# Performance work log

Hardware: AMD Instinct MI355X
Metric: run time of the kernel (lower is better)

The kernel has to match this reference:

```python
import math
import jax, jax.numpy as jnp
import numpy as np

NLAT, NLON = 61, 120
C, H = 64, 4
DH = C // H
HID = 128
NSEG = NLAT * NLON  # number of grid points / softmax segments
EPS = 1e-6
SCALE = 1.0 / math.sqrt(DH)


def _build_geometry():
    """Neighbor pairs within theta_cutoff on the equiangular (pole-including) grid.

    The neighborhood structure is longitude-shift invariant, so we enumerate it
    for output longitude 0 and replicate with a modular longitude shift.
    """
    nlat, nlon = NLAT, NLON
    theta = np.pi * np.arange(nlat) / (nlat - 1)           # colatitudes incl. poles
    lam = 2.0 * np.pi * np.arange(nlon) / nlon
    theta_cutoff = 7.0 / math.sqrt(math.pi) * math.pi / (nlat - 1)
    ct, st = np.cos(theta), np.sin(theta)
    # great-circle distance between (theta_o, 0) and (theta_i, dlon): [nlat, nlat, nlon]
    cosd = (ct[:, None, None] * ct[None, :, None]
            + st[:, None, None] * st[None, :, None] * np.cos(lam)[None, None, :])
    dist = np.arccos(np.clip(cosd, -1.0, 1.0))
    ho, hi, dl = np.nonzero(dist <= theta_cutoff)          # E reference-column entries
    wo = np.arange(nlon)
    out_idx = (ho[:, None] * nlon + wo[None, :]).reshape(-1).astype(np.int32)
    in_idx = (hi[:, None] * nlon + (dl[:, None] + wo[None, :]) % nlon).reshape(-1).astype(np.int32)
    # quadrature (integration) weights: sin(theta) measure, zero at the poles
    w = (st * (np.pi / (nlat - 1)) * (2.0 * np.pi / nlon)).astype(np.float32)
    quad_w = np.repeat(w, nlon)                            # [NSEG]
    return jnp.asarray(out_idx), jnp.asarray(in_idx), jnp.asarray(quad_w)


def setup_inputs() -> dict:
    key = jax.random.key(0)
    ks = jax.random.split(key, 8)
    out_idx, in_idx, quad_w = _build_geometry()

    def w(k, shape, fan_in):
        return jax.random.normal(k, shape, dtype=jnp.float32) / np.float32(np.sqrt(fan_in))

    return {
        "x": jax.random.normal(ks[0], (1, C, NLAT, NLON), dtype=jnp.float32),
        "wq": w(ks[1], (C, C), C),
        "wk": w(ks[2], (C, C), C),
        "wv": w(ks[3], (C, C), C),
        "wo": w(ks[4], (C, C), C),
        "w1": w(ks[5], (HID, C), C),
        "b1": jnp.zeros((HID,), jnp.float32),
        "w2": w(ks[6], (C, HID), HID),
        "b2": jnp.zeros((C,), jnp.float32),
        "ln0_g": jnp.ones((C,), jnp.float32),
        "ln0_b": jnp.zeros((C,), jnp.float32),
        "ln1_g": jnp.ones((C,), jnp.float32),
        "ln1_b": jnp.zeros((C,), jnp.float32),
        "quad_w": quad_w,
        "out_idx": out_idx,
        "in_idx": in_idx,
    }


def _layernorm(x, g, b):
    # channel-wise LayerNorm at every spatial location; x: [B, C, H, W]
    m = jnp.mean(x, axis=1, keepdims=True)
    v = jnp.mean((x - m) ** 2, axis=1, keepdims=True)
    xh = (x - m) * jax.lax.rsqrt(v + EPS)
    return xh * g[None, :, None, None] + b[None, :, None, None]


def _neighborhood_attn(x, wq, wk, wv, wo, quad_w, out_idx, in_idx):
    # x: [B, C, nlat, nlon] (fp32)
    B = x.shape[0]
    q = jnp.einsum('oc,bchw->bohw', wq, x).reshape(B, H, DH, NSEG)
    k = jnp.einsum('oc,bchw->bohw', wk, x).reshape(B, H, DH, NSEG)
    v = jnp.einsum('oc,bchw->bohw', wv, x).reshape(B, H, DH, NSEG)
    qg = q[..., out_idx]                                   # [B,H,DH,NNZ]
    kg = k[..., in_idx]
    s = jnp.einsum('bhdn,bhdn->bhn', qg, kg) * SCALE       # [B,H,NNZ]
    s = jnp.moveaxis(s, -1, 0)                             # [NNZ,B,H]
    smax = jax.ops.segment_max(s, out_idx, num_segments=NSEG)
    # quadrature-weighted, numerically stable softmax over each neighborhood
    alpha = jnp.exp(s - smax[out_idx]) * quad_w[in_idx][:, None, None]
    vg = jnp.moveaxis(v[..., in_idx], -1, 0)               # [NNZ,B,H,DH]
    num = jax.ops.segment_sum(alpha[..., None] * vg, out_idx, num_segments=NSEG)
    den = jax.ops.segment_sum(alpha, out_idx, num_segments=NSEG)
    att = num / den[..., None]                             # [NSEG,B,H,DH]
    att = jnp.moveaxis(att, 0, -1).reshape(B, C, NLAT, NLON)
    return jnp.einsum('oc,bchw->bohw', wo, att)


def reference(x, wq, wk, wv, wo, w1, b1, w2, b2, ln0_g, ln0_b, ln1_g, ln1_b,
              quad_w, out_idx, in_idx):
    residual = x
    h0 = _layernorm(x, ln0_g, ln0_b)
    a = _neighborhood_attn(h0.astype(jnp.float32), wq, wk, wv, wo,
                           quad_w, out_idx, in_idx).astype(x.dtype)
    x1 = a + residual
    h1 = _layernorm(x1, ln1_g, ln1_b)
    m = jax.nn.gelu(jnp.einsum('fc,bchw->bfhw', w1, h1) + b1[None, :, None, None],
                    approximate=False)
    m = jnp.einsum('cf,bfhw->bchw', w2, m) + b2[None, :, None, None]
    return m + x1
```

## Files before the change

### kernel.cpp

```cpp
#include <hip/hip_runtime.h>
#include <math.h>

#define NSEG 7320
#define NLON 120
#define HIDN 128
#define ZSPL 6
#define ECHUNK 8
#define NCHUNK 96

__global__ __launch_bounds__(256) void z0_zero(float4* __restrict__ p, int n4)
{
    int i = blockIdx.x * 256 + threadIdx.x;
    if (i < n4) p[i] = make_float4(0.f, 0.f, 0.f, 0.f);
}

__global__ __launch_bounds__(64) void k1_ln_qkv(
    const float* __restrict__ x,  const float* __restrict__ wq,
    const float* __restrict__ wk, const float* __restrict__ wv,
    const float* __restrict__ g,  const float* __restrict__ b,
    const int* __restrict__ out_idx, const int* __restrict__ in_idx,
    const float* __restrict__ qw, int E,
    float* __restrict__ q_pl, float* __restrict__ k_pl, float* __restrict__ v_pl,
    int* __restrict__ row_start, int4* __restrict__ meta)
{
    const int lane = threadIdx.x;
    const int tile = blockIdx.x;
    const int grp  = blockIdx.y;

    if (grp >= 24) {
        for (int e = tile * 64 + lane; e < E; e += 115 * 64) {
            int ho = out_idx[e * NLON] / NLON;
            if (e == 0) {
                row_start[ho] = 0;
            } else {
                int hp = out_idx[(e - 1) * NLON] / NLON;
                if (hp != ho) row_start[ho] = e;
            }
            if (e == E - 1) row_start[ho + 1] = E;
            int i0 = in_idx[e * NLON];
            int hi = i0 / NLON;
            int dl = i0 - hi * NLON;
            meta[e] = make_int4(hi * NLON, dl, __float_as_int(qw[i0]), ho);
        }
        return;
    }

    const int n = tile * 64 + lane;
    if (n >= NSEG) return;

    float xv[64];
    float s = 0.f, s2 = 0.f;
#pragma unroll
    for (int c = 0; c < 64; ++c) { float t = x[c * NSEG + n]; xv[c] = t; s += t; s2 += t * t; }
    float mean = s * 0.015625f;
    float var  = s2 * 0.015625f - mean * mean;
    float rstd = rsqrtf(var + 1e-6f);
#pragma unroll
    for (int c = 0; c < 64; ++c) xv[c] = (xv[c] - mean) * rstd * g[c] + b[c];

    const int mm    = grp >> 3;
    const int obase = (grp & 7) * 8;
    const float* __restrict__ w = (mm == 0) ? wq : (mm == 1) ? wk : wv;
    float* __restrict__ dst = (mm == 0) ? q_pl : (mm == 1) ? k_pl : v_pl;
    const float scale = (mm == 0) ? 0.25f : 1.0f;

#pragma unroll
    for (int j = 0; j < 8; ++j) {
        int o = obase + j;
        float acc = 0.f;
#pragma unroll
        for (int c = 0; c < 64; ++c) acc += w[o * 64 + c] * xv[c];
        dst[o * NSEG + n] = acc * scale;
    }
}

__global__ __launch_bounds__(128) void k2a_scores(
    const float* __restrict__ q_pl, const float* __restrict__ k_pl,
    const int4* __restrict__ meta,  const int* __restrict__ row_start,
    float* __restrict__ alpha, float* __restrict__ den, int E)
{
    const int wo  = threadIdx.x;
    const bool aw = wo < NLON;
    const int woc = aw ? wo : (NLON - 1);
    const int ho  = blockIdx.x;

    int e0 = __builtin_amdgcn_readfirstlane(row_start[ho]);
    int e1 = __builtin_amdgcn_readfirstlane(row_start[ho + 1]);
    int eb = e0 + blockIdx.y * ECHUNK;
    if (eb >= e1) return;
    int ee = eb + ECHUNK; if (ee > e1) ee = e1;

    const int segc = ho * NLON + woc;
    float qreg[64];
#pragma unroll
    for (int c = 0; c < 64; ++c) qreg[c] = q_pl[c * NSEG + segc];

    const size_t hstride = ((size_t)E) << 7;
    float dh0 = 0.f, dh1 = 0.f, dh2 = 0.f, dh3 = 0.f;

    for (int e = eb; e < ee; ++e) {
        int4 mt = meta[e];
        int dlw = mt.y + woc; if (dlw >= NLON) dlw -= NLON;
        int in  = mt.x + dlw;
        float s0 = 0.f, s1 = 0.f, s2 = 0.f, s3 = 0.f;
#pragma unroll
        for (int c = 0; c < 16; ++c) s0 += qreg[c]      * k_pl[c * NSEG + in];
#pragma unroll
        for (int c = 0; c < 16; ++c) s1 += qreg[16 + c] * k_pl[(16 + c) * NSEG + in];
#pragma unroll
        for (int c = 0; c < 16; ++c) s2 += qreg[32 + c] * k_pl[(32 + c) * NSEG + in];
#pragma unroll
        for (int c = 0; c < 16; ++c) s3 += qreg[48 + c] * k_pl[(48 + c) * NSEG + in];
        float qwv = aw ? __int_as_float(mt.z) : 0.f;
        float a0 = __expf(s0) * qwv, a1 = __expf(s1) * qwv;
        float a2 = __expf(s2) * qwv, a3 = __expf(s3) * qwv;
        dh0 += a0; dh1 += a1; dh2 += a2; dh3 += a3;
        if (aw) {
            size_t ab = (((size_t)e) << 7) + wo;
            alpha[ab]               = a0;
            alpha[hstride + ab]     = a1;
            alpha[2 * hstride + ab] = a2;
            alpha[3 * hstride + ab] = a3;
        }
    }
    if (aw) {
        int seg = ho * NLON + wo;
        atomicAdd(&den[0 * NSEG + seg], dh0);
        atomicAdd(&den[1 * NSEG + seg], dh1);
        atomicAdd(&den[2 * NSEG + seg], dh2);
        atomicAdd(&den[3 * NSEG + seg], dh3);
    }
}

__global__ __launch_bounds__(256) void k2b_pv(
    const float* __restrict__ v_pl, const int4* __restrict__ meta,
    const int* __restrict__ row_start, const float* __restrict__ alpha,
    float* __restrict__ num, int E)
{
    const int tid  = threadIdx.x;
    const int wv   = tid >> 6;
    const int lane = tid & 63;
    const int r    = blockIdx.x;
    const int ho   = (r & 1) ? (60 - (r >> 1)) : (r >> 1);
    const int c4   = blockIdx.y * 2 + (wv >> 1);
    const int half = wv & 1;
    const int wo   = half * 64 + lane;
    const bool aw  = wo < NLON;
    const int woc  = aw ? wo : (NLON - 1);
    const int head = c4 >> 2;
    const int c0   = c4 * 4;

    int e0 = __builtin_amdgcn_readfirstlane(row_start[ho]);
    int e1 = __builtin_amdgcn_readfirstlane(row_start[ho + 1]);
    int len = e1 - e0;
    int es = e0 + (len * (int)blockIdx.z) / ZSPL;
    int ef = e0 + (len * ((int)blockIdx.z + 1)) / ZSPL;

    const float* __restrict__ ah = alpha + ((((size_t)head) * E) << 7);
    const float* __restrict__ v0 = v_pl + (size_t)(c0 + 0) * NSEG;
    const float* __restrict__ v1 = v_pl + (size_t)(c0 + 1) * NSEG;
    const float* __restrict__ v2 = v_pl + (size_t)(c0 + 2) * NSEG;
    const float* __restrict__ v3 = v_pl + (size_t)(c0 + 3) * NSEG;

    float n0 = 0.f, n1 = 0.f, n2 = 0.f, n3 = 0.f;

    int e = es;
    for (; e + 4 <= ef; e += 4) {
        int4 ma = meta[e], mb = meta[e + 1], mc = meta[e + 2], md = meta[e + 3];
        int da = ma.y + woc; if (da >= NLON) da -= NLON;
        int db = mb.y + woc; if (db >= NLON) db -= NLON;
        int dc = mc.y + woc; if (dc >= NLON) dc -= NLON;
        int dd = md.y + woc; if (dd >= NLON) dd -= NLON;
        int ia = ma.x + da, ib = mb.x + db, ic = mc.x + dc, id = md.x + dd;
        float aa = ah[(((size_t)(e + 0)) << 7) + woc];
        float ab = ah[(((size_t)(e + 1)) << 7) + woc];
        float ac = ah[(((size_t)(e + 2)) << 7) + woc];
        float ad = ah[(((size_t)(e + 3)) << 7) + woc];
        float va0 = v0[ia], va1 = v1[ia], va2 = v2[ia], va3 = v3[ia];
        float vb0 = v0[ib], vb1 = v1[ib], vb2 = v2[ib], vb3 = v3[ib];
        float vc0 = v0[ic], vc1 = v1[ic], vc2 = v2[ic], vc3 = v3[ic];
        float vd0 = v0[id], vd1 = v1[id], vd2 = v2[id], vd3 = v3[id];
        n0 = fmaf(aa, va0, n0); n1 = fmaf(aa, va1, n1);
        n2 = fmaf(aa, va2, n2); n3 = fmaf(aa, va3, n3);
        n0 = fmaf(ab, vb0, n0); n1 = fmaf(ab, vb1, n1);
        n2 = fmaf(ab, vb2, n2); n3 = fmaf(ab, vb3, n3);
        n0 = fmaf(ac, vc0, n0); n1 = fmaf(ac, vc1, n1);
        n2 = fmaf(ac, vc2, n2); n3 = fmaf(ac, vc3, n3);
        n0 = fmaf(ad, vd0, n0); n1 = fmaf(ad, vd1, n1);
        n2 = fmaf(ad, vd2, n2); n3 = fmaf(ad, vd3, n3);
    }
    for (; e < ef; ++e) {
        int4 mt = meta[e];
        int dlw = mt.y + woc; if (dlw >= NLON) dlw -= NLON;
        int in  = mt.x + dlw;
        float a = ah[(((size_t)e) << 7) + woc];
        n0 = fmaf(a, v0[in], n0); n1 = fmaf(a, v1[in], n1);
        n2 = fmaf(a, v2[in], n2); n3 = fmaf(a, v3[in], n3);
    }

    if (aw) {
        int seg = ho * NLON + wo;
        atomicAdd(&num[(c0 + 0) * NSEG + seg], n0);
        atomicAdd(&num[(c0 + 1) * NSEG + seg], n1);
        atomicAdd(&num[(c0 + 2) * NSEG + seg], n2);
        atomicAdd(&num[(c0 + 3) * NSEG + seg], n3);
    }
}

__global__ __launch_bounds__(64) void k2c_wo(
    const float* __restrict__ num, const float* __restrict__ den,
    const float* __restrict__ wo,  const float* __restrict__ x,
    float* __restrict__ x1)
{
    const int lane = threadIdx.x;
    const int n    = blockIdx.x * 64 + lane;
    if (n >= NSEG) return;

    float rdh[4];
#pragma unroll
    for (int h = 0; h < 4; ++h) rdh[h] = 1.0f / den[h * NSEG + n];

    float att[64];
#pragma unroll
    for (int c = 0; c < 64; ++c) att[c] = num[c * NSEG + n] * rdh[c >> 4];

    const int o0 = blockIdx.y * 8;
#pragma unroll
    for (int j = 0; j < 8; ++j) {
        int o = o0 + j;
        float acc = 0.f;
#pragma unroll
        for (int c = 0; c < 64; ++c) acc += wo[o * 64 + c] * att[c];
        x1[o * NSEG + n] = acc + x[o * NSEG + n];
    }
}

__global__ __launch_bounds__(64) void k3a_mlp1(
    const float* __restrict__ x1, const float* __restrict__ w1,
    const float* __restrict__ b1, const float* __restrict__ g,
    const float* __restrict__ bb, float* __restrict__ m_act)
{
    const int lane = threadIdx.x;
    const int n    = blockIdx.x * 64 + lane;
    if (n >= NSEG) return;

    float xv[64];
    float s = 0.f, s2 = 0.f;
#pragma unroll
    for (int c = 0; c < 64; ++c) { float t = x1[c * NSEG + n]; xv[c] = t; s += t; s2 += t * t; }
    float mean = s * 0.015625f;
    float var  = s2 * 0.015625f - mean * mean;
    float rstd = rsqrtf(var + 1e-6f);
#pragma unroll
    for (int c = 0; c < 64; ++c) xv[c] = (xv[c] - mean) * rstd * g[c] + bb[c];

    const int h0 = blockIdx.y * 16;
#pragma unroll
    for (int j = 0; j < 16; ++j) {
        int h = h0 + j;
        float mh = b1[h];
#pragma unroll
        for (int c = 0; c < 64; ++c) mh += w1[h * 64 + c] * xv[c];
        m_act[h * NSEG + n] = 0.5f * mh * (1.0f + erff(mh * 0.70710678118654752f));
    }
}

__global__ __launch_bounds__(64) void k3b_mlp2(
    const float* __restrict__ m_act, const float* __restrict__ w2,
    const float* __restrict__ b2,    const float* __restrict__ x1,
    float* __restrict__ out)
{
    const int lane = threadIdx.x;
    const int n    = blockIdx.x * 64 + lane;
    if (n >= NSEG) return;
    const int c0   = blockIdx.y * 8;

    float acc[8];
#pragma unroll
    for (int j = 0; j < 8; ++j) acc[j] = 0.f;

#pragma unroll 8
    for (int h = 0; h < HIDN; ++h) {
        float mh = m_act[h * NSEG + n];
#pragma unroll
        for (int j = 0; j < 8; ++j) acc[j] += w2[(c0 + j) * HIDN + h] * mh;
    }
#pragma unroll
    for (int j = 0; j < 8; ++j) {
        int c = c0 + j;
        out[c * NSEG + n] = acc[j] + b2[c] + x1[c * NSEG + n];
    }
}

extern "C" void kernel_launch(void* const* d_in, const int* in_sizes, int n_in,
                              void* d_out, int out_size, void* d_ws, size_t ws_size,
                              hipStream_t stream)
{
    const float* x    = (const float*)d_in[0];
    const float* wq   = (const float*)d_in[1];
    const float* wk   = (const float*)d_in[2];
    const float* wv   = (const float*)d_in[3];
    const float* wo   = (const float*)d_in[4];
    const float* w1   = (const float*)d_in[5];
    const float* b1   = (const float*)d_in[6];
    const float* w2   = (const float*)d_in[7];
    const float* b2   = (const float*)d_in[8];
    const float* ln0g = (const float*)d_in[9];
    const float* ln0b = (const float*)d_in[10];
    const float* ln1g = (const float*)d_in[11];
    const float* ln1b = (const float*)d_in[12];
    const float* qw   = (const float*)d_in[13];
    const int* out_idx = (const int*)d_in[14];
    const int* in_idx  = (const int*)d_in[15];
    float* out = (float*)d_out;

    const int NNZ = in_sizes[15];
    const int E   = NNZ / NLON;
    const size_t N64 = (size_t)NSEG * 64;

    float* ws    = (float*)d_ws;
    float* q_pl  = ws;
    float* k_pl  = ws + N64;
    float* v_pl  = ws + 2 * N64;
    float* num   = ws + 3 * N64;
    float* den   = ws + 4 * N64;
    float* x1    = ws + 4 * N64 + 4 * NSEG;
    float* m_act = ws + 5 * N64 + 4 * NSEG;
    int*   row_start = (int*)(ws + 7 * N64 + 4 * NSEG);
    int4*  meta  = (int4*)(ws + 7 * N64 + 4 * NSEG + 64);
    float* alpha = ws + 7 * N64 + 4 * NSEG + 64 + 4 * (size_t)E;

    const int nz4 = (int)((68 * NSEG) / 4);
    hipLaunchKernelGGL(z0_zero, dim3((nz4 + 255) / 256), dim3(256), 0, stream,
                       (float4*)num, nz4);
    hipLaunchKernelGGL(k1_ln_qkv, dim3(115, 25), dim3(64), 0, stream,
                       x, wq, wk, wv, ln0g, ln0b, out_idx, in_idx, qw, E,
                       q_pl, k_pl, v_pl, row_start, meta);
    hipLaunchKernelGGL(k2a_scores, dim3(61, NCHUNK), dim3(128), 0, stream,
                       q_pl, k_pl, meta, row_start, alpha, den, E);
    hipLaunchKernelGGL(k2b_pv, dim3(61, 8, ZSPL), dim3(256), 0, stream,
                       v_pl, meta, row_start, alpha, num, E);
    hipLaunchKernelGGL(k2c_wo, dim3(115, 8), dim3(64), 0, stream,
                       num, den, wo, x, x1);
    hipLaunchKernelGGL(k3a_mlp1, dim3(115, 8), dim3(64), 0, stream,
                       x1, w1, b1, ln1g, ln1b, m_act);
    hipLaunchKernelGGL(k3b_mlp2, dim3(115, 8), dim3(64), 0, stream,
                       m_act, w2, b2, x1, out);
}
```

Baseline: 222.4 us.

## Fuse score and PV passes into one attention kernel, fold zeroing into QKV

Merges the score kernel and the PV kernel into one fused kernel. Each thread computes exp-weighted scores and accumulates alpha*V for all 64 channels in registers, so the large alpha buffer is no longer written and read back through global memory. The zero-fill kernel is folded into extra blocks of the QKV kernel, and the MLP1 grid is split finer (8 hidden units per block). The cost is higher register pressure from 128 live floats, 64 atomics per thread at the end, and fewer edge chunks per row. Correctness relies on the zeroing blocks in the same kernel finishing before k2_attn runs, which stream ordering guarantees.

```diff
diff --git a/kernel.cpp b/kernel.cpp
--- a/kernel.cpp
+++ b/kernel.cpp
@@ -4,15 +4,8 @@
 #define NSEG 7320
 #define NLON 120
 #define HIDN 128
-#define ZSPL 6
-#define ECHUNK 8
-#define NCHUNK 96
-
-__global__ __launch_bounds__(256) void z0_zero(float4* __restrict__ p, int n4)
-{
-    int i = blockIdx.x * 256 + threadIdx.x;
-    if (i < n4) p[i] = make_float4(0.f, 0.f, 0.f, 0.f);
-}
+#define ECH  16
+#define MAXCH 48
 
 __global__ __launch_bounds__(64) void k1_ln_qkv(
     const float* __restrict__ x,  const float* __restrict__ wq,
@@ -21,13 +14,20 @@
     const int* __restrict__ out_idx, const int* __restrict__ in_idx,
     const float* __restrict__ qw, int E,
     float* __restrict__ q_pl, float* __restrict__ k_pl, float* __restrict__ v_pl,
-    int* __restrict__ row_start, int4* __restrict__ meta)
+    int* __restrict__ row_start, int4* __restrict__ meta,
+    float4* __restrict__ zbase)
 {
     const int lane = threadIdx.x;
     const int tile = blockIdx.x;
     const int grp  = blockIdx.y;
 
-    if (grp >= 24) {
+    if (grp >= 25) {
+        const int n4 = (68 * NSEG) / 4;
+        for (int i = ((grp - 25) * 115 + tile) * 64 + lane; i < n4; i += 2 * 115 * 64)
+            zbase[i] = make_float4(0.f, 0.f, 0.f, 0.f);
+        return;
+    }
+    if (grp == 24) {
         for (int e = tile * 64 + lane; e < E; e += 115 * 64) {
             int ho = out_idx[e * NLON] / NLON;
             if (e == 0) {
@@ -74,10 +74,11 @@
     }
 }
 
-__global__ __launch_bounds__(128) void k2a_scores(
+__global__ __launch_bounds__(128) void k2_attn(
     const float* __restrict__ q_pl, const float* __restrict__ k_pl,
+    const float* __restrict__ v_pl,
     const int4* __restrict__ meta,  const int* __restrict__ row_start,
-    float* __restrict__ alpha, float* __restrict__ den, int E)
+    float* __restrict__ num, float* __restrict__ den)
 {
     const int wo  = threadIdx.x;
     const bool aw = wo < NLON;
@@ -86,45 +87,55 @@
 
     int e0 = __builtin_amdgcn_readfirstlane(row_start[ho]);
     int e1 = __builtin_amdgcn_readfirstlane(row_start[ho + 1]);
-    int eb = e0 + blockIdx.y * ECHUNK;
+    int eb = e0 + blockIdx.y * ECH;
     if (eb >= e1) return;
-    int ee = eb + ECHUNK; if (ee > e1) ee = e1;
+    int ee = eb + ECH; if (ee > e1) ee = e1;
 
     const int segc = ho * NLON + woc;
     float qreg[64];
 #pragma unroll
     for (int c = 0; c < 64; ++c) qreg[c] = q_pl[c * NSEG + segc];
 
-    const size_t hstride = ((size_t)E) << 7;
+    float acc[64];
+#pragma unroll
+    for (int c = 0; c < 64; ++c) acc[c] = 0.f;
     float dh0 = 0.f, dh1 = 0.f, dh2 = 0.f, dh3 = 0.f;
 
     for (int e = eb; e < ee; ++e) {
         int4 mt = meta[e];
         int dlw = mt.y + woc; if (dlw >= NLON) dlw -= NLON;
-        int in  = mt.x + dlw;
+        const float* __restrict__ kp = k_pl + (mt.x + dlw);
+        const float* __restrict__ vp = v_pl + (mt.x + dlw);
+
         float s0 = 0.f, s1 = 0.f, s2 = 0.f, s3 = 0.f;
 #pragma unroll
-        for (int c = 0; c < 16; ++c) s0 += qreg[c]      * k_pl[c * NSEG + in];
-#pragma unroll
-        for (int c = 0; c < 16; ++c) s1 += qreg[16 + c] * k_pl[(16 + c) * NSEG + in];
-#pragma unroll
-        for (int c = 0; c < 16; ++c) s2 += qreg[32 + c] * k_pl[(32 + c) * NSEG + in];
-#pragma unroll
-        for (int c = 0; c < 16; ++c) s3 += qreg[48 + c] * k_pl[(48 + c) * NSEG + in];
+        for (int c = 0; c < 16; ++c) s0 += qreg[c]      * kp[c * NSEG];
+#pragma unroll
+        for (int c = 0; c < 16; ++c) s1 += qreg[16 + c] * kp[(16 + c) * NSEG];
+#pragma unroll
+        for (int c = 0; c < 16; ++c) s2 += qreg[32 + c] * kp[(32 + c) * NSEG];
+#pragma unroll
+        for (int c = 0; c < 16; ++c) s3 += qreg[48 + c] * kp[(48 + c) * NSEG];
+
         float qwv = aw ? __int_as_float(mt.z) : 0.f;
         float a0 = __expf(s0) * qwv, a1 = __expf(s1) * qwv;
         float a2 = __expf(s2) * qwv, a3 = __expf(s3) * qwv;
         dh0 += a0; dh1 += a1; dh2 += a2; dh3 += a3;
-        if (aw) {
-            size_t ab = (((size_t)e) << 7) + wo;
-            alpha[ab]               = a0;
-            alpha[hstride + ab]     = a1;
-            alpha[2 * hstride + ab] = a2;
-            alpha[3 * hstride + ab] = a3;
-        }
-    }
+
+#pragma unroll
+        for (int c = 0; c < 16; ++c) acc[c]      = fmaf(a0, vp[c * NSEG],        acc[c]);
+#pragma unroll
+        for (int c = 0; c < 16; ++c) acc[16 + c] = fmaf(a1, vp[(16 + c) * NSEG], acc[16 + c]);
+#pragma unroll
+        for (int c = 0; c < 16; ++c) acc[32 + c] = fmaf(a2, vp[(32 + c) * NSEG], acc[32 + c]);
+#pragma unroll
+        for (int c = 0; c < 16; ++c) acc[48 + c] = fmaf(a3, vp[(48 + c) * NSEG], acc[48 + c]);
+    }
+
     if (aw) {
-        int seg = ho * NLON + wo;
+        const int seg = ho * NLON + wo;
+#pragma unroll
+        for (int c = 0; c < 64; ++c) atomicAdd(&num[c * NSEG + seg], acc[c]);
         atomicAdd(&den[0 * NSEG + seg], dh0);
         atomicAdd(&den[1 * NSEG + seg], dh1);
         atomicAdd(&den[2 * NSEG + seg], dh2);
@@ -132,81 +143,6 @@
     }
 }
 
-__global__ __launch_bounds__(256) void k2b_pv(
-    const float* __restrict__ v_pl, const int4* __restrict__ meta,
-    const int* __restrict__ row_start, const float* __restrict__ alpha,
-    float* __restrict__ num, int E)
-{
-    const int tid  = threadIdx.x;
-    const int wv   = tid >> 6;
-    const int lane = tid & 63;
-    const int r    = blockIdx.x;
-    const int ho   = (r & 1) ? (60 - (r >> 1)) : (r >> 1);
-    const int c4   = blockIdx.y * 2 + (wv >> 1);
-    const int half = wv & 1;
-    const int wo   = half * 64 + lane;
-    const bool aw  = wo < NLON;
-    const int woc  = aw ? wo : (NLON - 1);
-    const int head = c4 >> 2;
-    const int c0   = c4 * 4;
-
-    int e0 = __builtin_amdgcn_readfirstlane(row_start[ho]);
-    int e1 = __builtin_amdgcn_readfirstlane(row_start[ho + 1]);
-    int len = e1 - e0;
-    int es = e0 + (len * (int)blockIdx.z) / ZSPL;
-    int ef = e0 + (len * ((int)blockIdx.z + 1)) / ZSPL;
-
-    const float* __restrict__ ah = alpha + ((((size_t)head) * E) << 7);
-    const float* __restrict__ v0 = v_pl + (size_t)(c0 + 0) * NSEG;
-    const float* __restrict__ v1 = v_pl + (size_t)(c0 + 1) * NSEG;
-    const float* __restrict__ v2 = v_pl + (size_t)(c0 + 2) * NSEG;
-    const float* __restrict__ v3 = v_pl + (size_t)(c0 + 3) * NSEG;
-
-    float n0 = 0.f, n1 = 0.f, n2 = 0.f, n3 = 0.f;
-
-    int e = es;
-    for (; e + 4 <= ef; e += 4) {
-        int4 ma = meta[e], mb = meta[e + 1], mc = meta[e + 2], md = meta[e + 3];
-        int da = ma.y + woc; if (da >= NLON) da -= NLON;
-        int db = mb.y + woc; if (db >= NLON) db -= NLON;
-        int dc = mc.y + woc; if (dc >= NLON) dc -= NLON;
-        int dd = md.y + woc; if (dd >= NLON) dd -= NLON;
-        int ia = ma.x + da, ib = mb.x + db, ic = mc.x + dc, id = md.x + dd;
-        float aa = ah[(((size_t)(e + 0)) << 7) + woc];
-        float ab = ah[(((size_t)(e + 1)) << 7) + woc];
-        float ac = ah[(((size_t)(e + 2)) << 7) + woc];
-        float ad = ah[(((size_t)(e + 3)) << 7) + woc];
-        float va0 = v0[ia], va1 = v1[ia], va2 = v2[ia], va3 = v3[ia];
-        float vb0 = v0[ib], vb1 = v1[ib], vb2 = v2[ib], vb3 = v3[ib];
-        float vc0 = v0[ic], vc1 = v1[ic], vc2 = v2[ic], vc3 = v3[ic];
-        float vd0 = v0[id], vd1 = v1[id], vd2 = v2[id], vd3 = v3[id];
-        n0 = fmaf(aa, va0, n0); n1 = fmaf(aa, va1, n1);
-        n2 = fmaf(aa, va2, n2); n3 = fmaf(aa, va3, n3);
-        n0 = fmaf(ab, vb0, n0); n1 = fmaf(ab, vb1, n1);
-        n2 = fmaf(ab, vb2, n2); n3 = fmaf(ab, vb3, n3);
-        n0 = fmaf(ac, vc0, n0); n1 = fmaf(ac, vc1, n1);
-        n2 = fmaf(ac, vc2, n2); n3 = fmaf(ac, vc3, n3);
-        n0 = fmaf(ad, vd0, n0); n1 = fmaf(ad, vd1, n1);
-        n2 = fmaf(ad, vd2, n2); n3 = fmaf(ad, vd3, n3);
-    }
-    for (; e < ef; ++e) {
-        int4 mt = meta[e];
-        int dlw = mt.y + woc; if (dlw >= NLON) dlw -= NLON;
-        int in  = mt.x + dlw;
-        float a = ah[(((size_t)e) << 7) + woc];
-        n0 = fmaf(a, v0[in], n0); n1 = fmaf(a, v1[in], n1);
-        n2 = fmaf(a, v2[in], n2); n3 = fmaf(a, v3[in], n3);
-    }
-
-    if (aw) {
-        int seg = ho * NLON + wo;
-        atomicAdd(&num[(c0 + 0) * NSEG + seg], n0);
-        atomicAdd(&num[(c0 + 1) * NSEG + seg], n1);
-        atomicAdd(&num[(c0 + 2) * NSEG + seg], n2);
-        atomicAdd(&num[(c0 + 3) * NSEG + seg], n3);
-    }
-}
-
 __global__ __launch_bounds__(64) void k2c_wo(
     const float* __restrict__ num, const float* __restrict__ den,
     const float* __restrict__ wo,  const float* __restrict__ x,
@@ -254,9 +190,9 @@
 #pragma unroll
     for (int c = 0; c < 64; ++c) xv[c] = (xv[c] - mean) * rstd * g[c] + bb[c];
 
-    const int h0 = blockIdx.y * 16;
-#pragma unroll
-    for (int j = 0; j < 16; ++j) {
+    const int h0 = blockIdx.y * 8;
+#pragma unroll
+    for (int j = 0; j < 8; ++j) {
         int h = h0 + j;
         float mh = b1[h];
 #pragma unroll
@@ -328,21 +264,15 @@
     float* m_act = ws + 5 * N64 + 4 * NSEG;
     int*   row_start = (int*)(ws + 7 * N64 + 4 * NSEG);
     int4*  meta  = (int4*)(ws + 7 * N64 + 4 * NSEG + 64);
-    float* alpha = ws + 7 * N64 + 4 * NSEG + 64 + 4 * (size_t)E;
-
-    const int nz4 = (int)((68 * NSEG) / 4);
-    hipLaunchKernelGGL(z0_zero, dim3((nz4 + 255) / 256), dim3(256), 0, stream,
-                       (float4*)num, nz4);
-    hipLaunchKernelGGL(k1_ln_qkv, dim3(115, 25), dim3(64), 0, stream,
+
+    hipLaunchKernelGGL(k1_ln_qkv, dim3(115, 27), dim3(64), 0, stream,
                        x, wq, wk, wv, ln0g, ln0b, out_idx, in_idx, qw, E,
-                       q_pl, k_pl, v_pl, row_start, meta);
-    hipLaunchKernelGGL(k2a_scores, dim3(61, NCHUNK), dim3(128), 0, stream,
-                       q_pl, k_pl, meta, row_start, alpha, den, E);
-    hipLaunchKernelGGL(k2b_pv, dim3(61, 8, ZSPL), dim3(256), 0, stream,
-                       v_pl, meta, row_start, alpha, num, E);
+                       q_pl, k_pl, v_pl, row_start, meta, (float4*)num);
+    hipLaunchKernelGGL(k2_attn, dim3(61, MAXCH), dim3(128), 0, stream,
+                       q_pl, k_pl, v_pl, meta, row_start, num, den);
     hipLaunchKernelGGL(k2c_wo, dim3(115, 8), dim3(64), 0, stream,
                        num, den, wo, x, x1);
-    hipLaunchKernelGGL(k3a_mlp1, dim3(115, 8), dim3(64), 0, stream,
+    hipLaunchKernelGGL(k3a_mlp1, dim3(115, 16), dim3(64), 0, stream,
                        x1, w1, b1, ln1g, ln1b, m_act);
     hipLaunchKernelGGL(k3b_mlp2, dim3(115, 8), dim3(64), 0, stream,
                        m_act, w2, b2, x1, out);
```

Result: slower. 307.4 us (+38.2%).
